# Kernel optimization log

Measured on AMD Instinct MI355X. Metric: run time of the kernel, lower is better.

Reference implementation:

```python
import jax, jax.numpy as jnp
import numpy as np
from jax.scipy.special import logsumexp

GRID_N = 512
N_ITERS = 5


def _build_grid(n):
    nH = n * (n - 1)
    E = 2 * n * (n - 1)
    P = (n - 1) * (n - 1)
    N = n * n
    pi, pj = np.meshgrid(np.arange(n - 1), np.arange(n - 1), indexing='ij')
    pi, pj = pi.ravel(), pj.ravel()
    # child edges of plaquette (i,j): top/bottom horizontal, left/right vertical
    pce = np.stack([pi * (n - 1) + pj,
                    (pi + 1) * (n - 1) + pj,
                    nH + pi * n + pj,
                    nH + pi * n + pj + 1], 1).astype(np.int32)
    epp = np.zeros((E, 2), np.int32)
    eps = np.zeros((E, 2), np.int32)
    epm = np.zeros((E, 2), np.float32)
    ev = np.zeros((E, 2), np.int32)
    hi, hj = np.meshgrid(np.arange(n), np.arange(n - 1), indexing='ij')
    hi, hj = hi.ravel(), hj.ravel()
    he = hi * (n - 1) + hj
    m = hi < n - 1
    epp[he[m], 0] = hi[m] * (n - 1) + hj[m]; epm[he[m], 0] = 1; eps[he, 0] = 0
    m = hi > 0
    epp[he[m], 1] = (hi[m] - 1) * (n - 1) + hj[m]; epm[he[m], 1] = 1; eps[he, 1] = 1
    ev[he, 0] = hi * n + hj; ev[he, 1] = hi * n + hj + 1
    vi, vj = np.meshgrid(np.arange(n - 1), np.arange(n), indexing='ij')
    vi, vj = vi.ravel(), vj.ravel()
    ve = nH + vi * n + vj
    m = vj < n - 1
    epp[ve[m], 0] = vi[m] * (n - 1) + vj[m]; epm[ve[m], 0] = 1; eps[ve, 0] = 2
    m = vj > 0
    epp[ve[m], 1] = vi[m] * (n - 1) + vj[m] - 1; epm[ve[m], 1] = 1; eps[ve, 1] = 3
    ev[ve, 0] = vi * n + vj; ev[ve, 1] = (vi + 1) * n + vj
    return epp, eps, epm, pce, ev, E, P, N


def setup_inputs() -> dict:
    n = GRID_N
    epp, eps, epm, pce, ev, E, P, N = _build_grid(n)
    key = jax.random.key(0)
    k1, k2 = jax.random.split(key)
    return {
        'log_phi_plaq': 0.5 * jax.random.normal(k1, (P, 2, 2, 2, 2), jnp.float32),
        'log_phi_edge': 0.5 * jax.random.normal(k2, (E, 2, 2), jnp.float32),
        'edge_parent_plaq': jnp.asarray(epp),
        'edge_parent_slot': jnp.asarray(eps),
        'edge_parent_mask': jnp.asarray(epm),
        'plaq_child_edge': jnp.asarray(pce),
        'edge_vars': jnp.asarray(ev),
        'n_iters': N_ITERS,
        'n_vars': N,
    }


def _forward(log_phi_plaq, log_phi_edge, epp, eps, epm, pce, ev, n_iters, n_vars):
    P = log_phi_plaq.shape[0]
    maskNN = epm[:, :, None, None]

    def edge_totals(logM):
        # sum of log-messages from (<=2) parents into each edge, plus edge factor
        g = logM[epp, eps]                      # [E,2,2,2]
        return log_phi_edge + jnp.sum(g * maskNN, axis=1)  # [E,2,2]

    def plaq_terms(logM, tot):
        n_all = tot[pce] - logM                 # [P,4,2,2]: child msg excluding this parent
        b0 = n_all[:, 0, :, :, None, None]      # top edge -> vars (a,b)
        b1 = n_all[:, 1, None, None, :, :]      # bottom  -> vars (c,d)
        b2 = n_all[:, 2, :, None, :, None]      # left    -> vars (a,c)
        b3 = n_all[:, 3, None, :, None, :]      # right   -> vars (b,d)
        S = log_phi_plaq + b0 + b1 + b2 + b3    # [P,2,2,2,2] plaquette log-belief (unnorm)
        return S, (b0, b1, b2, b3)

    def step(logM, _):
        tot = edge_totals(logM)
        S, (b0, b1, b2, b3) = plaq_terms(logM, tot)
        m0 = logsumexp(S - b0, axis=(3, 4))
        m1 = logsumexp(S - b1, axis=(1, 2))
        m2 = logsumexp(S - b2, axis=(2, 4))
        m3 = logsumexp(S - b3, axis=(1, 3))
        new = jnp.stack([m0, m1, m2, m3], axis=1)
        new = new - logsumexp(new, axis=(2, 3), keepdims=True)  # normalize messages
        return new, None

    logM0 = jnp.full((P, 4, 2, 2), -jnp.log(4.0), log_phi_plaq.dtype)
    logM, _ = jax.lax.scan(step, logM0, None, length=n_iters)

    tot = edge_totals(logM)
    log_b_e = tot - logsumexp(tot, axis=(1, 2), keepdims=True)
    S, _ = plaq_terms(logM, tot)
    log_b_p = S - logsumexp(S, axis=(1, 2, 3, 4), keepdims=True)
    b_e = jnp.exp(log_b_e)
    b_p = jnp.exp(log_b_p)

    # Kikuchi free energy: c_plaq = 1, c_edge = 1 - #parents
    c_e = 1.0 - jnp.sum(epm, axis=1)
    F = (jnp.sum(b_p * (log_b_p - log_phi_plaq))
         + jnp.sum(c_e * jnp.sum(b_e * (log_b_e - log_phi_edge), axis=(1, 2))))

    binary_marginals = b_e                      # every pair is an R1 region
    pa = b_e.sum(axis=2)                        # [E,2] marginal of first var
    pb = b_e.sum(axis=1)                        # [E,2] marginal of second var
    ones = jnp.ones((ev.shape[0],), b_e.dtype)
    node_sum = (jax.ops.segment_sum(pa, ev[:, 0], num_segments=n_vars)
                + jax.ops.segment_sum(pb, ev[:, 1], num_segments=n_vars))
    deg = (jax.ops.segment_sum(ones, ev[:, 0], num_segments=n_vars)
           + jax.ops.segment_sum(ones, ev[:, 1], num_segments=n_vars))
    unary_marginals = node_sum / deg[:, None]   # [N,2]
    return -F, unary_marginals, binary_marginals


def reference(log_phi_plaq, log_phi_edge, edge_parent_plaq, edge_parent_slot,
              edge_parent_mask, plaq_child_edge, edge_vars, n_iters, n_vars):
    return _forward(log_phi_plaq, log_phi_edge, edge_parent_plaq, edge_parent_slot,
                    edge_parent_mask, plaq_child_edge, edge_vars, n_iters, n_vars)
```

## Files before the change

### kernel.cpp

```cpp
#include <hip/hip_runtime.h>
#include <hip/hip_fp16.h>
#include <math.h>


#define CORE 22
#define REG  32
#define NTHR 512
#define QC   2

static __device__ __forceinline__ float4 ld4(const float* p){ return *(const float4*)p; }
static __device__ __forceinline__ float rcpf(float x){ return __builtin_amdgcn_rcpf(x); }
static __device__ __forceinline__ void up4(const __half2* p, int s, float* d){
  __half2 a = p[2*s], b = p[2*s+1];
  d[0]=__low2float(a); d[1]=__high2float(a); d[2]=__low2float(b); d[3]=__high2float(b);
}

__global__ __launch_bounds__(NTHR, 2)
void fused_kernel(const float* __restrict__ phiP, const float* __restrict__ phiE,
                  float* __restrict__ outBin, float* __restrict__ Pblk,
                  int m, int n)
{
  __shared__ __half2 pln[2][8][REG*REG];
  const int t = threadIdx.x;
  const int base_i = (int)blockIdx.y*CORE - 5;
  const int base_j = (int)blockIdx.x*CORE - 5;
  const int nH = n*m;

  __half2 peH[QC][8], phH[QC][8];
  #pragma unroll
  for (int q=0; q<QC; ++q){
    const int r  = t + q*NTHR;
    const int ry = r >> 5, rx = r & 31;
    const int gi = base_i + ry, gj = base_j + rx;
    const int ci = min(max(gi,0), m-1), cj = min(max(gj,0), m-1);
    float4 v;
    v = ld4(phiE + 4*(size_t)(ci*m+cj));
    peH[q][0]=__floats2half2_rn(__expf(v.x),__expf(v.y));
    peH[q][1]=__floats2half2_rn(__expf(v.z),__expf(v.w));
    v = ld4(phiE + 4*(size_t)((ci+1)*m+cj));
    peH[q][2]=__floats2half2_rn(__expf(v.x),__expf(v.y));
    peH[q][3]=__floats2half2_rn(__expf(v.z),__expf(v.w));
    v = ld4(phiE + 4*(size_t)(nH+ci*n+cj));
    peH[q][4]=__floats2half2_rn(__expf(v.x),__expf(v.y));
    peH[q][5]=__floats2half2_rn(__expf(v.z),__expf(v.w));
    v = ld4(phiE + 4*(size_t)(nH+ci*n+cj+1));
    peH[q][6]=__floats2half2_rn(__expf(v.x),__expf(v.y));
    peH[q][7]=__floats2half2_rn(__expf(v.z),__expf(v.w));
    const float* pp = phiP + 16*(size_t)(ci*m+cj);
    #pragma unroll
    for (int h=0; h<4; ++h){
      v = ld4(pp + 4*h);
      phH[q][2*h+0]=__floats2half2_rn(__expf(v.x),__expf(v.y));
      phH[q][2*h+1]=__floats2half2_rn(__expf(v.z),__expf(v.w));
    }
  }

  for (int it=0; it<5; ++it){
    const int cb = it & 1, nb = cb ^ 1;
    #pragma unroll
    for (int q=0; q<QC; ++q){
      const int r  = t + q*NTHR;
      const int ry = r >> 5, rx = r & 31;
      const int gi = base_i + ry, gj = base_j + rx;
      const bool m0 = gi > 0, m1 = gi < m-1, m2 = gj > 0, m3 = gj < m-1;
      const int r0 = max(ry-1,0)*REG + rx;
      const int r1 = min(ry+1,REG-1)*REG + rx;
      const int r2 = ry*REG + max(rx-1,0);
      const int r3 = ry*REG + min(rx+1,REG-1);

      float pe[16];
      up4(peH[q],0,pe+0); up4(peH[q],1,pe+4); up4(peH[q],2,pe+8); up4(peH[q],3,pe+12);

      float na[4][4];
      if (it == 0){
        #pragma unroll
        for (int k=0;k<16;k++) na[k>>2][k&3] = pe[k];
      } else {
        __half2 a, b; float4 o;
        const float4 one = make_float4(1.f,1.f,1.f,1.f);
        a = pln[cb][2][r0]; b = pln[cb][3][r0];
        o = m0 ? make_float4(__low2float(a),__high2float(a),__low2float(b),__high2float(b)) : one;
        na[0][0]=pe[0]*o.x; na[0][1]=pe[1]*o.y; na[0][2]=pe[2]*o.z; na[0][3]=pe[3]*o.w;
        a = pln[cb][0][r1]; b = pln[cb][1][r1];
        o = m1 ? make_float4(__low2float(a),__high2float(a),__low2float(b),__high2float(b)) : one;
        na[1][0]=pe[4]*o.x; na[1][1]=pe[5]*o.y; na[1][2]=pe[6]*o.z; na[1][3]=pe[7]*o.w;
        a = pln[cb][6][r2]; b = pln[cb][7][r2];
        o = m2 ? make_float4(__low2float(a),__high2float(a),__low2float(b),__high2float(b)) : one;
        na[2][0]=pe[8]*o.x; na[2][1]=pe[9]*o.y; na[2][2]=pe[10]*o.z; na[2][3]=pe[11]*o.w;
        a = pln[cb][4][r3]; b = pln[cb][5][r3];
        o = m3 ? make_float4(__low2float(a),__high2float(a),__low2float(b),__high2float(b)) : one;
        na[3][0]=pe[12]*o.x; na[3][1]=pe[13]*o.y; na[3][2]=pe[14]*o.z; na[3][3]=pe[15]*o.w;
      }

      float ph[16];
      up4(phH[q],0,ph+0); up4(phH[q],1,ph+4); up4(phH[q],2,ph+8); up4(phH[q],3,ph+12);

      float g[4][4];
      #pragma unroll
      for (int s=0;s<4;s++){ g[s][0]=0.f; g[s][1]=0.f; g[s][2]=0.f; g[s][3]=0.f; }
      #pragma unroll
      for (int idx=0; idx<16; ++idx){
        const int a=(idx>>3)&1, b=(idx>>2)&1, c=(idx>>1)&1, d=idx&1;
        const int ab=(a<<1)|b, cd=(c<<1)|d, ac=(a<<1)|c, bd=(b<<1)|d;
        float E = (na[0][ab]*na[1][cd]) * (na[2][ac]*na[3][bd]) * ph[idx];
        g[0][ab]+=E; g[1][cd]+=E; g[2][ac]+=E; g[3][bd]+=E;
      }
      #pragma unroll
      for (int s=0;s<4;s++){
        float l1=na[s][0], l2=l1*na[s][1], l3=l2*na[s][2];
        float q2=na[s][3], q1=q2*na[s][2], q0=q1*na[s][1];
        float o0=g[s][0]*q0, o1=g[s][1]*l1*q1, o2=g[s][2]*l2*q2, o3=g[s][3]*l3;
        float inv = rcpf(fmaxf(fmaxf(o0,o1), fmaxf(o2,o3)));
        pln[nb][2*s+0][r] = __floats2half2_rn(o0*inv, o1*inv);
        pln[nb][2*s+1][r] = __floats2half2_rn(o2*inv, o3*inv);
      }
    }
    __syncthreads();
  }

  float contrib = 0.f;
  #pragma unroll
  for (int q=0; q<QC; ++q){
    const int r  = t + q*NTHR;
    const int ry = r >> 5, rx = r & 31;
    const int gi = base_i + ry, gj = base_j + rx;
    const bool core = (ry >= 5) && (ry < 5+CORE) && (gi < m) &&
                      (rx >= 5) && (rx < 5+CORE) && (gj < m);
    if (!core) continue;
    const bool m0 = gi > 0, m1 = gi < m-1, m2 = gj > 0, m3 = gj < m-1;
    const int r0 = max(ry-1,0)*REG + rx;
    const int r1 = min(ry+1,REG-1)*REG + rx;
    const int r2 = ry*REG + max(rx-1,0);
    const int r3 = ry*REG + min(rx+1,REG-1);

    float pe[16], ph[16], own[16];
    up4(peH[q],0,pe+0); up4(peH[q],1,pe+4); up4(peH[q],2,pe+8); up4(peH[q],3,pe+12);
    up4(phH[q],0,ph+0); up4(phH[q],1,ph+4); up4(phH[q],2,ph+8); up4(phH[q],3,ph+12);
    #pragma unroll
    for (int h=0; h<8; ++h){
      __half2 a = pln[1][h][r];
      own[2*h]=__low2float(a); own[2*h+1]=__high2float(a);
    }

    float o5_0[4], o5_2[4], naE5[4][4];
    {
      __half2 a, b; float4 o;
      const float4 one = make_float4(1.f,1.f,1.f,1.f);
      a = pln[1][2][r0]; b = pln[1][3][r0];
      o = m0 ? make_float4(__low2float(a),__high2float(a),__low2float(b),__high2float(b)) : one;
      o5_0[0]=o.x; o5_0[1]=o.y; o5_0[2]=o.z; o5_0[3]=o.w;
      naE5[0][0]=pe[0]*o.x; naE5[0][1]=pe[1]*o.y; naE5[0][2]=pe[2]*o.z; naE5[0][3]=pe[3]*o.w;
      a = pln[1][0][r1]; b = pln[1][1][r1];
      o = m1 ? make_float4(__low2float(a),__high2float(a),__low2float(b),__high2float(b)) : one;
      naE5[1][0]=pe[4]*o.x; naE5[1][1]=pe[5]*o.y; naE5[1][2]=pe[6]*o.z; naE5[1][3]=pe[7]*o.w;
      a = pln[1][6][r2]; b = pln[1][7][r2];
      o = m2 ? make_float4(__low2float(a),__high2float(a),__low2float(b),__high2float(b)) : one;
      o5_2[0]=o.x; o5_2[1]=o.y; o5_2[2]=o.z; o5_2[3]=o.w;
      naE5[2][0]=pe[8]*o.x; naE5[2][1]=pe[9]*o.y; naE5[2][2]=pe[10]*o.z; naE5[2][3]=pe[11]*o.w;
      a = pln[1][4][r3]; b = pln[1][5][r3];
      o = m3 ? make_float4(__low2float(a),__high2float(a),__low2float(b),__high2float(b)) : one;
      naE5[3][0]=pe[12]*o.x; naE5[3][1]=pe[13]*o.y; naE5[3][2]=pe[14]*o.z; naE5[3][3]=pe[15]*o.w;
    }
    {
      float Ln[4][4];
      #pragma unroll
      for (int s=0;s<4;s++)
        #pragma unroll
        for (int k=0;k<4;k++)
          Ln[s][k] = __logf(fmaxf(naE5[s][k], 1e-30f));
      float Z=0.f, accT=0.f;
      #pragma unroll
      for (int idx=0; idx<16; ++idx){
        const int a=(idx>>3)&1, b=(idx>>2)&1, c=(idx>>1)&1, d=idx&1;
        const int ab=(a<<1)|b, cd=(c<<1)|d, ac=(a<<1)|c, bd=(b<<1)|d;
        float E = (naE5[0][ab]*naE5[1][cd]) * (naE5[2][ac]*naE5[3][bd]) * ph[idx];
        float T = (Ln[0][ab]+Ln[1][cd]) + (Ln[2][ac]+Ln[3][bd]);
        Z += E; accT = fmaf(E, T, accT);
      }
      contrib += accT*rcpf(Z) - __logf(Z);
    }
    {
      float P0=naE5[0][0]*own[0], P1=naE5[0][1]*own[1],
            P2=naE5[0][2]*own[2], P3=naE5[0][3]*own[3];
      float Zt=P0+P1+P2+P3, izt=rcpf(Zt);
      float* ob = outBin + 4*(size_t)(gi*m+gj);
      ob[0]=P0*izt; ob[1]=P1*izt; ob[2]=P2*izt; ob[3]=P3*izt;
      if (gi>0){
        float q0=__logf(fmaxf(o5_0[0]*own[0],1e-30f));
        float q1=__logf(fmaxf(o5_0[1]*own[1],1e-30f));
        float q2=__logf(fmaxf(o5_0[2]*own[2],1e-30f));
        float q3=__logf(fmaxf(o5_0[3]*own[3],1e-30f));
        contrib += __logf(Zt) - (P0*q0+P1*q1+P2*q2+P3*q3)*izt;
      }
    }
    {
      float P0=naE5[2][0]*own[8],  P1=naE5[2][1]*own[9],
            P2=naE5[2][2]*own[10], P3=naE5[2][3]*own[11];
      float Zt=P0+P1+P2+P3, izt=rcpf(Zt);
      float* ob = outBin + 4*(size_t)(nH+gi*n+gj);
      ob[0]=P0*izt; ob[1]=P1*izt; ob[2]=P2*izt; ob[3]=P3*izt;
      if (gj>0){
        float q0=__logf(fmaxf(o5_2[0]*own[8], 1e-30f));
        float q1=__logf(fmaxf(o5_2[1]*own[9], 1e-30f));
        float q2=__logf(fmaxf(o5_2[2]*own[10],1e-30f));
        float q3=__logf(fmaxf(o5_2[3]*own[11],1e-30f));
        contrib += __logf(Zt) - (P0*q0+P1*q1+P2*q2+P3*q3)*izt;
      }
    }
    if (gi == m-1){
      float P0=naE5[1][0]*own[4], P1=naE5[1][1]*own[5],
            P2=naE5[1][2]*own[6], P3=naE5[1][3]*own[7];
      float izt=rcpf(P0+P1+P2+P3);
      float* ob = outBin + 4*(size_t)((gi+1)*m+gj);
      ob[0]=P0*izt; ob[1]=P1*izt; ob[2]=P2*izt; ob[3]=P3*izt;
    }
    if (gj == m-1){
      float P0=naE5[3][0]*own[12], P1=naE5[3][1]*own[13],
            P2=naE5[3][2]*own[14], P3=naE5[3][3]*own[15];
      float izt=rcpf(P0+P1+P2+P3);
      float* ob = outBin + 4*(size_t)(nH+gi*n+gj+1);
      ob[0]=P0*izt; ob[1]=P1*izt; ob[2]=P2*izt; ob[3]=P3*izt;
    }
  }

  __syncthreads();
  float* red = (float*)&pln[0][0][0];
  #pragma unroll
  for (int off=32; off>0; off>>=1) contrib += __shfl_down(contrib, off, 64);
  if ((t & 63) == 0) red[t >> 6] = contrib;
  __syncthreads();
  if (t < 8){
    float v = red[t];
    #pragma unroll
    for (int off=4; off>0; off>>=1) v += __shfl_down(v, off, 8);
    if (t == 0) Pblk[blockIdx.y*gridDim.x + blockIdx.x] = v;
  }
}

__global__ __launch_bounds__(256)
void unary_kernel(const float* __restrict__ bin, float* __restrict__ out,
                  const float* __restrict__ Pblk, int m, int n, int nblk)
{
  if (blockIdx.x == 0 && blockIdx.y == 0){
    __shared__ float red[256];
    int tid = threadIdx.y*64 + threadIdx.x;
    float s = 0.f;
    for (int idx = tid; idx < nblk; idx += 256) s += Pblk[idx];
    red[tid] = s; __syncthreads();
    #pragma unroll
    for (int st=128; st>0; st>>=1){
      if (tid < st) red[tid] += red[tid+st];
      __syncthreads();
    }
    if (tid == 0) out[0] = -red[0];
  }
  int j = blockIdx.x*64 + threadIdx.x;
  int i = blockIdx.y*4  + threadIdx.y;
  if (i >= n || j >= n) return;
  const int nH = n*m;
  float s0=0.f, s1=0.f, deg=0.f;
  if (j < m){ const float* b = bin + 4*(size_t)(i*m+j);        s0 += b[0]+b[1]; s1 += b[2]+b[3]; deg+=1.f; }
  if (j > 0){ const float* b = bin + 4*(size_t)(i*m+j-1);      s0 += b[0]+b[2]; s1 += b[1]+b[3]; deg+=1.f; }
  if (i < m){ const float* b = bin + 4*(size_t)(nH+i*n+j);     s0 += b[0]+b[1]; s1 += b[2]+b[3]; deg+=1.f; }
  if (i > 0){ const float* b = bin + 4*(size_t)(nH+(i-1)*n+j); s0 += b[0]+b[2]; s1 += b[1]+b[3]; deg+=1.f; }
  float inv = 1.f/deg;
  size_t v = (size_t)i*n + j;
  out[1+2*v]   = s0*inv;
  out[1+2*v+1] = s1*inv;
}

extern "C" void kernel_launch(void* const* d_in, const int* in_sizes, int n_in,
                              void* d_out, int out_size, void* d_ws, size_t ws_size,
                              hipStream_t stream)
{
  const float* phiP = (const float*)d_in[0];
  const float* phiE = (const float*)d_in[1];
  int P  = in_sizes[0] / 16;
  int m  = (int)(sqrt((double)P) + 0.5);
  int n  = m + 1;
  int N  = n * n;
  float* out  = (float*)d_out;
  float* Pblk = (float*)d_ws;

  int tiles = (m + CORE - 1) / CORE;
  float* outBin = out + 1 + 2*(size_t)N;
  fused_kernel<<<dim3(tiles, tiles), dim3(NTHR), 0, stream>>>(phiP, phiE, outBin, Pblk, m, n);
  unary_kernel<<<dim3((n+63)/64, (n+3)/4), dim3(64,4), 0, stream>>>(outBin, out, Pblk, m, n, tiles*tiles);
}
```

Before: 144.8 us.

## Enlarge core tile to 32 with a 42x42 region and interleave shared message planes

Each block now owns a 32x32 core plus a 5-cell halo (a 42x42 region) instead of 22x22 inside 32x32. That cuts the fraction of redundant halo belief-propagation work and shrinks the grid to 16x16 blocks, which matches the CU count. Shared messages are stored interleaved per cell, so each neighbour read fetches both half2 values together. In exchange the index math uses a non-power-of-two divide and the tile needs about 113KB of LDS, allowing only one block per CU. The higher launch-bounds block count may also force register pressure or spills.

```diff
diff --git a/kernel.cpp b/kernel.cpp
--- a/kernel.cpp
+++ b/kernel.cpp
@@ -3,55 +3,65 @@
 #include <math.h>
 
 
-#define CORE 22
-#define REG  32
-#define NTHR 512
-#define QC   2
+#define HALO  5
+#define CORE  32
+#define RW    (CORE + 2*HALO)
+#define NCELL (RW*RW)
+#define NTHR  896
+#define QC    2
 
 static __device__ __forceinline__ float4 ld4(const float* p){ return *(const float4*)p; }
 static __device__ __forceinline__ float rcpf(float x){ return __builtin_amdgcn_rcpf(x); }
-static __device__ __forceinline__ void up4(const __half2* p, int s, float* d){
+
+static __device__ __forceinline__ void rd4(const __half2 (*pl)[2], int r, bool msk, float* o){
+  __half2 a = pl[r][0], b = pl[r][1];
+  float x0=__low2float(a), x1=__high2float(a), x2=__low2float(b), x3=__high2float(b);
+  o[0]=msk?x0:1.f; o[1]=msk?x1:1.f; o[2]=msk?x2:1.f; o[3]=msk?x3:1.f;
+}
+static __device__ __forceinline__ void up4h(const __half2* p, int s, float* d){
   __half2 a = p[2*s], b = p[2*s+1];
   d[0]=__low2float(a); d[1]=__high2float(a); d[2]=__low2float(b); d[3]=__high2float(b);
 }
 
-__global__ __launch_bounds__(NTHR, 2)
+__global__ __launch_bounds__(NTHR, 4)
 void fused_kernel(const float* __restrict__ phiP, const float* __restrict__ phiE,
                   float* __restrict__ outBin, float* __restrict__ Pblk,
                   int m, int n)
 {
-  __shared__ __half2 pln[2][8][REG*REG];
+  __shared__ __half2 pln[2][4][NCELL][2];
   const int t = threadIdx.x;
-  const int base_i = (int)blockIdx.y*CORE - 5;
-  const int base_j = (int)blockIdx.x*CORE - 5;
+  const int base_i = (int)blockIdx.y*CORE - HALO;
+  const int base_j = (int)blockIdx.x*CORE - HALO;
   const int nH = n*m;
 
   __half2 peH[QC][8], phH[QC][8];
   #pragma unroll
   for (int q=0; q<QC; ++q){
-    const int r  = t + q*NTHR;
-    const int ry = r >> 5, rx = r & 31;
-    const int gi = base_i + ry, gj = base_j + rx;
-    const int ci = min(max(gi,0), m-1), cj = min(max(gj,0), m-1);
-    float4 v;
-    v = ld4(phiE + 4*(size_t)(ci*m+cj));
-    peH[q][0]=__floats2half2_rn(__expf(v.x),__expf(v.y));
-    peH[q][1]=__floats2half2_rn(__expf(v.z),__expf(v.w));
-    v = ld4(phiE + 4*(size_t)((ci+1)*m+cj));
-    peH[q][2]=__floats2half2_rn(__expf(v.x),__expf(v.y));
-    peH[q][3]=__floats2half2_rn(__expf(v.z),__expf(v.w));
-    v = ld4(phiE + 4*(size_t)(nH+ci*n+cj));
-    peH[q][4]=__floats2half2_rn(__expf(v.x),__expf(v.y));
-    peH[q][5]=__floats2half2_rn(__expf(v.z),__expf(v.w));
-    v = ld4(phiE + 4*(size_t)(nH+ci*n+cj+1));
-    peH[q][6]=__floats2half2_rn(__expf(v.x),__expf(v.y));
-    peH[q][7]=__floats2half2_rn(__expf(v.z),__expf(v.w));
-    const float* pp = phiP + 16*(size_t)(ci*m+cj);
-    #pragma unroll
-    for (int h=0; h<4; ++h){
-      v = ld4(pp + 4*h);
-      phH[q][2*h+0]=__floats2half2_rn(__expf(v.x),__expf(v.y));
-      phH[q][2*h+1]=__floats2half2_rn(__expf(v.z),__expf(v.w));
+    const int r = t + q*NTHR;
+    if (r < NCELL){
+      const int ry = r / RW, rx = r - ry*RW;
+      const int gi = base_i + ry, gj = base_j + rx;
+      const int ci = min(max(gi,0), m-1), cj = min(max(gj,0), m-1);
+      float4 v;
+      v = ld4(phiE + 4*(size_t)(ci*m+cj));
+      peH[q][0]=__floats2half2_rn(__expf(v.x),__expf(v.y));
+      peH[q][1]=__floats2half2_rn(__expf(v.z),__expf(v.w));
+      v = ld4(phiE + 4*(size_t)((ci+1)*m+cj));
+      peH[q][2]=__floats2half2_rn(__expf(v.x),__expf(v.y));
+      peH[q][3]=__floats2half2_rn(__expf(v.z),__expf(v.w));
+      v = ld4(phiE + 4*(size_t)(nH+ci*n+cj));
+      peH[q][4]=__floats2half2_rn(__expf(v.x),__expf(v.y));
+      peH[q][5]=__floats2half2_rn(__expf(v.z),__expf(v.w));
+      v = ld4(phiE + 4*(size_t)(nH+ci*n+cj+1));
+      peH[q][6]=__floats2half2_rn(__expf(v.x),__expf(v.y));
+      peH[q][7]=__floats2half2_rn(__expf(v.z),__expf(v.w));
+      const float* pp = phiP + 16*(size_t)(ci*m+cj);
+      #pragma unroll
+      for (int h=0; h<4; ++h){
+        v = ld4(pp + 4*h);
+        phH[q][2*h+0]=__floats2half2_rn(__expf(v.x),__expf(v.y));
+        phH[q][2*h+1]=__floats2half2_rn(__expf(v.z),__expf(v.w));
+      }
     }
   }
 
@@ -59,133 +69,128 @@
     const int cb = it & 1, nb = cb ^ 1;
     #pragma unroll
     for (int q=0; q<QC; ++q){
-      const int r  = t + q*NTHR;
-      const int ry = r >> 5, rx = r & 31;
-      const int gi = base_i + ry, gj = base_j + rx;
-      const bool m0 = gi > 0, m1 = gi < m-1, m2 = gj > 0, m3 = gj < m-1;
-      const int r0 = max(ry-1,0)*REG + rx;
-      const int r1 = min(ry+1,REG-1)*REG + rx;
-      const int r2 = ry*REG + max(rx-1,0);
-      const int r3 = ry*REG + min(rx+1,REG-1);
-
-      float pe[16];
-      up4(peH[q],0,pe+0); up4(peH[q],1,pe+4); up4(peH[q],2,pe+8); up4(peH[q],3,pe+12);
-
-      float na[4][4];
-      if (it == 0){
-        #pragma unroll
-        for (int k=0;k<16;k++) na[k>>2][k&3] = pe[k];
-      } else {
-        __half2 a, b; float4 o;
-        const float4 one = make_float4(1.f,1.f,1.f,1.f);
-        a = pln[cb][2][r0]; b = pln[cb][3][r0];
-        o = m0 ? make_float4(__low2float(a),__high2float(a),__low2float(b),__high2float(b)) : one;
-        na[0][0]=pe[0]*o.x; na[0][1]=pe[1]*o.y; na[0][2]=pe[2]*o.z; na[0][3]=pe[3]*o.w;
-        a = pln[cb][0][r1]; b = pln[cb][1][r1];
-        o = m1 ? make_float4(__low2float(a),__high2float(a),__low2float(b),__high2float(b)) : one;
-        na[1][0]=pe[4]*o.x; na[1][1]=pe[5]*o.y; na[1][2]=pe[6]*o.z; na[1][3]=pe[7]*o.w;
-        a = pln[cb][6][r2]; b = pln[cb][7][r2];
-        o = m2 ? make_float4(__low2float(a),__high2float(a),__low2float(b),__high2float(b)) : one;
-        na[2][0]=pe[8]*o.x; na[2][1]=pe[9]*o.y; na[2][2]=pe[10]*o.z; na[2][3]=pe[11]*o.w;
-        a = pln[cb][4][r3]; b = pln[cb][5][r3];
-        o = m3 ? make_float4(__low2float(a),__high2float(a),__low2float(b),__high2float(b)) : one;
-        na[3][0]=pe[12]*o.x; na[3][1]=pe[13]*o.y; na[3][2]=pe[14]*o.z; na[3][3]=pe[15]*o.w;
-      }
-
-      float ph[16];
-      up4(phH[q],0,ph+0); up4(phH[q],1,ph+4); up4(phH[q],2,ph+8); up4(phH[q],3,ph+12);
-
-      float g[4][4];
+      const int r = t + q*NTHR;
+      if (r < NCELL){
+        const int ry = r / RW, rx = r - ry*RW;
+        const int gi = base_i + ry, gj = base_j + rx;
+        const bool m0 = gi > 0, m1 = gi < m-1, m2 = gj > 0, m3 = gj < m-1;
+
+        float pe[16];
+        up4h(peH[q],0,pe+0); up4h(peH[q],1,pe+4);
+        up4h(peH[q],2,pe+8); up4h(peH[q],3,pe+12);
+
+        float na[4][4];
+        if (it == 0){
+          #pragma unroll
+          for (int k=0;k<16;++k) na[k>>2][k&3] = pe[k];
+        } else {
+          const int r0 = max(ry-1,0)*RW + rx;
+          const int r1 = min(ry+1,RW-1)*RW + rx;
+          const int r2 = ry*RW + max(rx-1,0);
+          const int r3 = ry*RW + min(rx+1,RW-1);
+          float o[4];
+          rd4(pln[cb][1], r0, m0, o);
+          na[0][0]=pe[0]*o[0]; na[0][1]=pe[1]*o[1]; na[0][2]=pe[2]*o[2]; na[0][3]=pe[3]*o[3];
+          rd4(pln[cb][0], r1, m1, o);
+          na[1][0]=pe[4]*o[0]; na[1][1]=pe[5]*o[1]; na[1][2]=pe[6]*o[2]; na[1][3]=pe[7]*o[3];
+          rd4(pln[cb][3], r2, m2, o);
+          na[2][0]=pe[8]*o[0]; na[2][1]=pe[9]*o[1]; na[2][2]=pe[10]*o[2]; na[2][3]=pe[11]*o[3];
+          rd4(pln[cb][2], r3, m3, o);
+          na[3][0]=pe[12]*o[0]; na[3][1]=pe[13]*o[1]; na[3][2]=pe[14]*o[2]; na[3][3]=pe[15]*o[3];
+        }
+
+        float ph[16];
+        up4h(phH[q],0,ph+0); up4h(phH[q],1,ph+4);
+        up4h(phH[q],2,ph+8); up4h(phH[q],3,ph+12);
+
+        float g[4][4];
+        #pragma unroll
+        for (int s=0;s<4;++s){ g[s][0]=0.f; g[s][1]=0.f; g[s][2]=0.f; g[s][3]=0.f; }
+        #pragma unroll
+        for (int idx=0; idx<16; ++idx){
+          const int a=(idx>>3)&1, b=(idx>>2)&1, c=(idx>>1)&1, d=idx&1;
+          const int ab=(a<<1)|b, cd=(c<<1)|d, ac=(a<<1)|c, bd=(b<<1)|d;
+          float E = (na[0][ab]*na[1][cd]) * (na[2][ac]*na[3][bd]) * ph[idx];
+          g[0][ab]+=E; g[1][cd]+=E; g[2][ac]+=E; g[3][bd]+=E;
+        }
+        #pragma unroll
+        for (int s=0;s<4;++s){
+          float l1=na[s][0], l2=l1*na[s][1], l3=l2*na[s][2];
+          float q2=na[s][3], q1=q2*na[s][2], q0=q1*na[s][1];
+          float o0=g[s][0]*q0, o1=g[s][1]*l1*q1, o2=g[s][2]*l2*q2, o3=g[s][3]*l3;
+          float inv = rcpf(fmaxf(fmaxf(o0,o1), fmaxf(o2,o3)));
+          pln[nb][s][r][0] = __floats2half2_rn(o0*inv, o1*inv);
+          pln[nb][s][r][1] = __floats2half2_rn(o2*inv, o3*inv);
+        }
+      }
+    }
+    __syncthreads();
+  }
+
+  float contrib = 0.f;
+  #pragma unroll
+  for (int q=0; q<QC; ++q){
+    const int r = t + q*NTHR;
+    if (r >= NCELL) continue;
+    const int ry = r / RW, rx = r - ry*RW;
+    const int gi = base_i + ry, gj = base_j + rx;
+    const bool core = (ry >= HALO) && (ry < HALO+CORE) && (gi < m) &&
+                      (rx >= HALO) && (rx < HALO+CORE) && (gj < m);
+    if (!core) continue;
+    const bool m0 = gi > 0, m1 = gi < m-1, m2 = gj > 0, m3 = gj < m-1;
+    const int r0 = r - RW, r1 = r + RW, r2 = r - 1, r3 = r + 1;
+
+    float pe[16], ph[16], own[16];
+    up4h(peH[q],0,pe+0); up4h(peH[q],1,pe+4);
+    up4h(peH[q],2,pe+8); up4h(peH[q],3,pe+12);
+    up4h(phH[q],0,ph+0); up4h(phH[q],1,ph+4);
+    up4h(phH[q],2,ph+8); up4h(phH[q],3,ph+12);
+    #pragma unroll
+    for (int s=0;s<4;++s){
+      __half2 a = pln[1][s][r][0], b = pln[1][s][r][1];
+      own[4*s+0]=__low2float(a); own[4*s+1]=__high2float(a);
+      own[4*s+2]=__low2float(b); own[4*s+3]=__high2float(b);
+    }
+
+    float o5_0[4], o5_2[4], na[4][4];
+    {
+      float o[4];
+      rd4(pln[1][1], r0, m0, o5_0);
+      na[0][0]=pe[0]*o5_0[0]; na[0][1]=pe[1]*o5_0[1];
+      na[0][2]=pe[2]*o5_0[2]; na[0][3]=pe[3]*o5_0[3];
+      rd4(pln[1][0], r1, m1, o);
+      na[1][0]=pe[4]*o[0]; na[1][1]=pe[5]*o[1]; na[1][2]=pe[6]*o[2]; na[1][3]=pe[7]*o[3];
+      rd4(pln[1][3], r2, m2, o5_2);
+      na[2][0]=pe[8]*o5_2[0];  na[2][1]=pe[9]*o5_2[1];
+      na[2][2]=pe[10]*o5_2[2]; na[2][3]=pe[11]*o5_2[3];
+      rd4(pln[1][2], r3, m3, o);
+      na[3][0]=pe[12]*o[0]; na[3][1]=pe[13]*o[1]; na[3][2]=pe[14]*o[2]; na[3][3]=pe[15]*o[3];
+    }
+    {
+      float Ln[4][4];
       #pragma unroll
-      for (int s=0;s<4;s++){ g[s][0]=0.f; g[s][1]=0.f; g[s][2]=0.f; g[s][3]=0.f; }
+      for (int s=0;s<4;++s)
+        #pragma unroll
+        for (int k=0;k<4;++k)
+          Ln[s][k] = __logf(fmaxf(na[s][k], 1e-30f));
+      float Z=0.f, accT=0.f;
       #pragma unroll
       for (int idx=0; idx<16; ++idx){
         const int a=(idx>>3)&1, b=(idx>>2)&1, c=(idx>>1)&1, d=idx&1;
         const int ab=(a<<1)|b, cd=(c<<1)|d, ac=(a<<1)|c, bd=(b<<1)|d;
         float E = (na[0][ab]*na[1][cd]) * (na[2][ac]*na[3][bd]) * ph[idx];
-        g[0][ab]+=E; g[1][cd]+=E; g[2][ac]+=E; g[3][bd]+=E;
-      }
-      #pragma unroll
-      for (int s=0;s<4;s++){
-        float l1=na[s][0], l2=l1*na[s][1], l3=l2*na[s][2];
-        float q2=na[s][3], q1=q2*na[s][2], q0=q1*na[s][1];
-        float o0=g[s][0]*q0, o1=g[s][1]*l1*q1, o2=g[s][2]*l2*q2, o3=g[s][3]*l3;
-        float inv = rcpf(fmaxf(fmaxf(o0,o1), fmaxf(o2,o3)));
-        pln[nb][2*s+0][r] = __floats2half2_rn(o0*inv, o1*inv);
-        pln[nb][2*s+1][r] = __floats2half2_rn(o2*inv, o3*inv);
-      }
-    }
-    __syncthreads();
-  }
-
-  float contrib = 0.f;
-  #pragma unroll
-  for (int q=0; q<QC; ++q){
-    const int r  = t + q*NTHR;
-    const int ry = r >> 5, rx = r & 31;
-    const int gi = base_i + ry, gj = base_j + rx;
-    const bool core = (ry >= 5) && (ry < 5+CORE) && (gi < m) &&
-                      (rx >= 5) && (rx < 5+CORE) && (gj < m);
-    if (!core) continue;
-    const bool m0 = gi > 0, m1 = gi < m-1, m2 = gj > 0, m3 = gj < m-1;
-    const int r0 = max(ry-1,0)*REG + rx;
-    const int r1 = min(ry+1,REG-1)*REG + rx;
-    const int r2 = ry*REG + max(rx-1,0);
-    const int r3 = ry*REG + min(rx+1,REG-1);
-
-    float pe[16], ph[16], own[16];
-    up4(peH[q],0,pe+0); up4(peH[q],1,pe+4); up4(peH[q],2,pe+8); up4(peH[q],3,pe+12);
-    up4(phH[q],0,ph+0); up4(phH[q],1,ph+4); up4(phH[q],2,ph+8); up4(phH[q],3,ph+12);
-    #pragma unroll
-    for (int h=0; h<8; ++h){
-      __half2 a = pln[1][h][r];
-      own[2*h]=__low2float(a); own[2*h+1]=__high2float(a);
-    }
-
-    float o5_0[4], o5_2[4], naE5[4][4];
-    {
-      __half2 a, b; float4 o;
-      const float4 one = make_float4(1.f,1.f,1.f,1.f);
-      a = pln[1][2][r0]; b = pln[1][3][r0];
-      o = m0 ? make_float4(__low2float(a),__high2float(a),__low2float(b),__high2float(b)) : one;
-      o5_0[0]=o.x; o5_0[1]=o.y; o5_0[2]=o.z; o5_0[3]=o.w;
-      naE5[0][0]=pe[0]*o.x; naE5[0][1]=pe[1]*o.y; naE5[0][2]=pe[2]*o.z; naE5[0][3]=pe[3]*o.w;
-      a = pln[1][0][r1]; b = pln[1][1][r1];
-      o = m1 ? make_float4(__low2float(a),__high2float(a),__low2float(b),__high2float(b)) : one;
-      naE5[1][0]=pe[4]*o.x; naE5[1][1]=pe[5]*o.y; naE5[1][2]=pe[6]*o.z; naE5[1][3]=pe[7]*o.w;
-      a = pln[1][6][r2]; b = pln[1][7][r2];
-      o = m2 ? make_float4(__low2float(a),__high2float(a),__low2float(b),__high2float(b)) : one;
-      o5_2[0]=o.x; o5_2[1]=o.y; o5_2[2]=o.z; o5_2[3]=o.w;
-      naE5[2][0]=pe[8]*o.x; naE5[2][1]=pe[9]*o.y; naE5[2][2]=pe[10]*o.z; naE5[2][3]=pe[11]*o.w;
-      a = pln[1][4][r3]; b = pln[1][5][r3];
-      o = m3 ? make_float4(__low2float(a),__high2float(a),__low2float(b),__high2float(b)) : one;
-      naE5[3][0]=pe[12]*o.x; naE5[3][1]=pe[13]*o.y; naE5[3][2]=pe[14]*o.z; naE5[3][3]=pe[15]*o.w;
-    }
-    {
-      float Ln[4][4];
-      #pragma unroll
-      for (int s=0;s<4;s++)
-        #pragma unroll
-        for (int k=0;k<4;k++)
-          Ln[s][k] = __logf(fmaxf(naE5[s][k], 1e-30f));
-      float Z=0.f, accT=0.f;
-      #pragma unroll
-      for (int idx=0; idx<16; ++idx){
-        const int a=(idx>>3)&1, b=(idx>>2)&1, c=(idx>>1)&1, d=idx&1;
-        const int ab=(a<<1)|b, cd=(c<<1)|d, ac=(a<<1)|c, bd=(b<<1)|d;
-        float E = (naE5[0][ab]*naE5[1][cd]) * (naE5[2][ac]*naE5[3][bd]) * ph[idx];
         float T = (Ln[0][ab]+Ln[1][cd]) + (Ln[2][ac]+Ln[3][bd]);
         Z += E; accT = fmaf(E, T, accT);
       }
       contrib += accT*rcpf(Z) - __logf(Z);
     }
     {
-      float P0=naE5[0][0]*own[0], P1=naE5[0][1]*own[1],
-            P2=naE5[0][2]*own[2], P3=naE5[0][3]*own[3];
+      float P0=na[0][0]*own[0], P1=na[0][1]*own[1],
+            P2=na[0][2]*own[2], P3=na[0][3]*own[3];
       float Zt=P0+P1+P2+P3, izt=rcpf(Zt);
       float* ob = outBin + 4*(size_t)(gi*m+gj);
       ob[0]=P0*izt; ob[1]=P1*izt; ob[2]=P2*izt; ob[3]=P3*izt;
-      if (gi>0){
+      if (m0){
         float q0=__logf(fmaxf(o5_0[0]*own[0],1e-30f));
         float q1=__logf(fmaxf(o5_0[1]*own[1],1e-30f));
         float q2=__logf(fmaxf(o5_0[2]*own[2],1e-30f));
@@ -194,12 +199,12 @@
       }
     }
     {
-      float P0=naE5[2][0]*own[8],  P1=naE5[2][1]*own[9],
-            P2=naE5[2][2]*own[10], P3=naE5[2][3]*own[11];
+      float P0=na[2][0]*own[8],  P1=na[2][1]*own[9],
+            P2=na[2][2]*own[10], P3=na[2][3]*own[11];
       float Zt=P0+P1+P2+P3, izt=rcpf(Zt);
       float* ob = outBin + 4*(size_t)(nH+gi*n+gj);
       ob[0]=P0*izt; ob[1]=P1*izt; ob[2]=P2*izt; ob[3]=P3*izt;
-      if (gj>0){
+      if (m2){
         float q0=__logf(fmaxf(o5_2[0]*own[8], 1e-30f));
         float q1=__logf(fmaxf(o5_2[1]*own[9], 1e-30f));
         float q2=__logf(fmaxf(o5_2[2]*own[10],1e-30f));
@@ -208,15 +213,15 @@
       }
     }
     if (gi == m-1){
-      float P0=naE5[1][0]*own[4], P1=naE5[1][1]*own[5],
-            P2=naE5[1][2]*own[6], P3=naE5[1][3]*own[7];
+      float P0=na[1][0]*own[4], P1=na[1][1]*own[5],
+            P2=na[1][2]*own[6], P3=na[1][3]*own[7];
       float izt=rcpf(P0+P1+P2+P3);
       float* ob = outBin + 4*(size_t)((gi+1)*m+gj);
       ob[0]=P0*izt; ob[1]=P1*izt; ob[2]=P2*izt; ob[3]=P3*izt;
     }
     if (gj == m-1){
-      float P0=naE5[3][0]*own[12], P1=naE5[3][1]*own[13],
-            P2=naE5[3][2]*own[14], P3=naE5[3][3]*own[15];
+      float P0=na[3][0]*own[12], P1=na[3][1]*own[13],
+            P2=na[3][2]*own[14], P3=na[3][3]*own[15];
       float izt=rcpf(P0+P1+P2+P3);
       float* ob = outBin + 4*(size_t)(nH+gi*n+gj+1);
       ob[0]=P0*izt; ob[1]=P1*izt; ob[2]=P2*izt; ob[3]=P3*izt;
@@ -224,15 +229,15 @@
   }
 
   __syncthreads();
-  float* red = (float*)&pln[0][0][0];
+  float* red = (float*)&pln[0][0][0][0];
   #pragma unroll
   for (int off=32; off>0; off>>=1) contrib += __shfl_down(contrib, off, 64);
   if ((t & 63) == 0) red[t >> 6] = contrib;
   __syncthreads();
-  if (t < 8){
-    float v = red[t];
-    #pragma unroll
-    for (int off=4; off>0; off>>=1) v += __shfl_down(v, off, 8);
+  if (t < 16){
+    float v = (t < NTHR/64) ? red[t] : 0.f;
+    #pragma unroll
+    for (int off=8; off>0; off>>=1) v += __shfl_down(v, off, 16);
     if (t == 0) Pblk[blockIdx.y*gridDim.x + blockIdx.x] = v;
   }
 }
```

Measured after the change: 141.3 us. 1.02x faster.
